# Kernel optimization log

Hardware: AMD Instinct MI355X
Metric: run time of the kernel (lower is better)

The kernel has to match this reference:

```python
import jax, jax.numpy as jnp
import numpy as np

B, S, H = 4, 2048, 2048
E, K = 8, 2


def setup_inputs() -> dict:
    key = jax.random.key(0)
    k1, k2, k3 = jax.random.split(key, 3)
    hidden_states = jax.random.normal(k1, (B, S, H), dtype=jnp.float32)
    # torch nn.Linear weight layout: [out_features, in_features]
    gate_w = jax.random.normal(k2, (E, H), dtype=jnp.float32) * (1.0 / np.sqrt(H))
    expert_w = jax.random.normal(k3, (E, H, H), dtype=jnp.float32) * (1.0 / np.sqrt(H))
    return {"hidden_states": hidden_states, "gate_w": gate_w, "expert_w": expert_w}


def reference(hidden_states, gate_w, expert_w):
    b, s, h = hidden_states.shape
    x = hidden_states.reshape(-1, h)                      # [T, H]
    T = x.shape[0]
    router_logits = x @ gate_w.T                          # [T, E]
    probs = jax.nn.softmax(router_logits.astype(jnp.float32), axis=-1)
    topk_w, topk_idx = jax.lax.top_k(probs, K)            # [T, K]
    topk_w = topk_w / jnp.sum(topk_w, axis=-1, keepdims=True)  # norm_topk_prob
    topk_w = topk_w.astype(x.dtype)
    # dense combine weights: cw[t, e] = sum_k topk_w[t, k] * (topk_idx[t, k] == e)
    cw = jnp.zeros((T, E), dtype=x.dtype).at[jnp.arange(T)[:, None], topk_idx].add(topk_w)
    # per-expert outputs: expert e computes x @ W_e^T  (W_e is [out, in])
    expert_out = jnp.einsum('th,edh->ted', x, expert_w)   # [T, E, H]
    out = jnp.einsum('ted,te->td', expert_out, cw)        # [T, H]
    return out.reshape(b, s, h), router_logits
```

## Files before the change

### kernel.cpp

```cpp
#include <hip/hip_runtime.h>
#include <hip/hip_bf16.h>

#define T_TOK 8192
#define H_DIM 2048
#define NE 8

typedef float f32x4 __attribute__((ext_vector_type(4)));
typedef short s16x8 __attribute__((ext_vector_type(8)));

typedef __attribute__((address_space(3))) unsigned int lds_uint;
typedef __attribute__((address_space(1))) const unsigned int glob_uint;

static __device__ __forceinline__ void async_ld16(const void* g, void* l) {
    __builtin_amdgcn_global_load_lds((glob_uint*)g, (lds_uint*)l, 16, 0, 0);
}

static __device__ __forceinline__ unsigned short f32_to_bf16(float f) {
    unsigned int u = __builtin_bit_cast(unsigned int, f);
    unsigned int r = (u + 0x7FFFu + ((u >> 16) & 1u)) >> 16;
    return (unsigned short)r;
}

__global__ __launch_bounds__(256) void prep_kernel(
        const float* __restrict__ w, unsigned short* __restrict__ wb,
        int* __restrict__ cnt) {
    const long g = (long)blockIdx.x * 256 + threadIdx.x;
    if (g < NE) cnt[g] = 0;
    const long nt = (long)gridDim.x * 256;
    const long N_W4 = (long)NE * H_DIM * H_DIM / 4;
    const float4* w4 = (const float4*)w;
    ushort4* wb4 = (ushort4*)wb;
    for (long i = g; i < N_W4; i += nt) {
        float4 v = w4[i];
        wb4[i] = make_ushort4(f32_to_bf16(v.x), f32_to_bf16(v.y),
                              f32_to_bf16(v.z), f32_to_bf16(v.w));
    }
}

__global__ __launch_bounds__(256) void router_kernel(
        const float* __restrict__ x, const float* __restrict__ gate,
        unsigned short* __restrict__ xb, float* __restrict__ logits,
        int* __restrict__ cnt, int* __restrict__ list, float* __restrict__ wl) {
    __shared__ float4 gs[NE * H_DIM / 4];
    __shared__ int aExp[32];
    __shared__ float aW[32];
    const float4* g4 = (const float4*)gate;
    for (int i = threadIdx.x; i < NE * H_DIM / 4; i += 256) gs[i] = g4[i];
    __syncthreads();

    const int wave = threadIdx.x >> 6, lane = threadIdx.x & 63;

    for (int it = 0; it < 4; ++it) {
        const int tok = wave * 4 + it;
        const int t = blockIdx.x * 16 + tok;
        const float4* xr = (const float4*)(x + (long)t * H_DIM);
        ushort4* xw = (ushort4*)(xb + (long)t * H_DIM);
        float acc[NE];
#pragma unroll
        for (int e = 0; e < NE; ++e) acc[e] = 0.f;
#pragma unroll
        for (int i = 0; i < 8; ++i) {
            float4 xv = xr[i * 64 + lane];
            xw[i * 64 + lane] = make_ushort4(f32_to_bf16(xv.x), f32_to_bf16(xv.y),
                                             f32_to_bf16(xv.z), f32_to_bf16(xv.w));
#pragma unroll
            for (int e = 0; e < NE; ++e) {
                float4 gv = gs[e * 512 + i * 64 + lane];
                acc[e] += xv.x * gv.x + xv.y * gv.y + xv.z * gv.z + xv.w * gv.w;
            }
        }
#pragma unroll
        for (int e = 0; e < NE; ++e)
#pragma unroll
            for (int off = 32; off > 0; off >>= 1)
                acc[e] += __shfl_xor(acc[e], off, 64);

        if (lane == 0) {
            float l0 = -1e30f; int i0 = 0;
#pragma unroll
            for (int e = 0; e < NE; ++e)
                if (acc[e] > l0) { l0 = acc[e]; i0 = e; }
            float l1 = -1e30f; int i1 = 0;
#pragma unroll
            for (int e = 0; e < NE; ++e)
                if (e != i0 && acc[e] > l1) { l1 = acc[e]; i1 = e; }
            float e1v = __expf(l1 - l0);
            float inv = 1.f / (1.f + e1v);
#pragma unroll
            for (int e = 0; e < NE; ++e) logits[(long)t * NE + e] = acc[e];
            aExp[tok * 2] = i0;     aW[tok * 2] = inv;
            aExp[tok * 2 + 1] = i1; aW[tok * 2 + 1] = e1v * inv;
        }
    }
    __syncthreads();

    if (threadIdx.x < NE) {
        const int e = threadIdx.x;
        int c = 0;
#pragma unroll
        for (int k = 0; k < 32; ++k) c += (aExp[k] == e);
        if (c) {
            int pos = atomicAdd(&cnt[e], c);
            for (int k = 0; k < 32; ++k)
                if (aExp[k] == e) {
                    list[e * T_TOK + pos] = blockIdx.x * 16 + (k >> 1);
                    wl[e * T_TOK + pos] = aW[k];
                    ++pos;
                }
        }
    }
}

__global__ __launch_bounds__(256, 4) void moe_gemm(
        const unsigned short* __restrict__ xb, const unsigned short* __restrict__ wb,
        const int* __restrict__ cnt, const int* __restrict__ list,
        const float* __restrict__ wl, float* __restrict__ out) {
    __shared__ uint4 As[1024];
    __shared__ uint4 Bs[1024];
    __shared__ int tIdx[128];
    __shared__ float tw[128];

    const int bx = blockIdx.x;
    const int e  = bx >> 10;
    const int rt = (bx >> 4) & 63;
    const int ct = bx & 15;
    const int n = cnt[e];
    const int row0 = rt << 7;
    if (row0 >= n) return;
    const int rv = min(128, n - row0);

    const int tid = threadIdx.x;
    if (tid < 128) {
        if (tid < rv) {
            tIdx[tid] = list[e * T_TOK + row0 + tid];
            tw[tid]   = wl[e * T_TOK + row0 + tid];
        } else { tIdx[tid] = 0; tw[tid] = 0.f; }
    }
    __syncthreads();

    const int wave = tid >> 6, lane = tid & 63;
    const int wm = (wave >> 1) << 6;
    const int wn = (wave & 1) << 6;
    const int quad = lane >> 4, l16 = lane & 15;

    f32x4 acc[4][4];
#pragma unroll
    for (int i = 0; i < 4; ++i)
#pragma unroll
        for (int j = 0; j < 4; ++j) acc[i][j] = (f32x4){0.f, 0.f, 0.f, 0.f};

    const unsigned short* aSrc[4];
    const unsigned short* bSrc[4];
    const long wbase = (long)e * H_DIM * H_DIM + (long)(ct * 128) * H_DIM;
#pragma unroll
    for (int i = 0; i < 4; ++i) {
        const int p = i * 256 + wave * 64 + lane;
        const int r = p >> 3;
        const int c = (p & 7) ^ (r & 7);
        aSrc[i] = xb + (long)tIdx[r] * H_DIM + c * 8;
        bSrc[i] = wb + wbase + (long)r * H_DIM + c * 8;
    }

    for (int kt = 0; kt < H_DIM / 64; ++kt) {
        const int k0 = kt * 64;
#pragma unroll
        for (int i = 0; i < 4; ++i) {
            async_ld16(aSrc[i] + k0, &As[i * 256 + wave * 64]);
            async_ld16(bSrc[i] + k0, &Bs[i * 256 + wave * 64]);
        }
        __syncthreads();
#pragma unroll
        for (int ks = 0; ks < 2; ++ks) {
            s16x8 af[4], bfr[4];
            const int kc = ks * 4 + quad;
#pragma unroll
            for (int i = 0; i < 4; ++i) {
                int r = wm + i * 16 + l16;
                af[i] = ((const s16x8*)As)[(r << 3) | (kc ^ (r & 7))];
            }
#pragma unroll
            for (int j = 0; j < 4; ++j) {
                int d = wn + j * 16 + l16;
                bfr[j] = ((const s16x8*)Bs)[(d << 3) | (kc ^ (d & 7))];
            }
#pragma unroll
            for (int i = 0; i < 4; ++i)
#pragma unroll
                for (int j = 0; j < 4; ++j)
                    acc[i][j] = __builtin_amdgcn_mfma_f32_16x16x32_bf16(
                        af[i], bfr[j], acc[i][j], 0, 0, 0);
        }
        __syncthreads();
    }

    const int colbase = ct * 128 + wn;
#pragma unroll
    for (int i = 0; i < 4; ++i) {
        const int rbase = wm + i * 16 + quad * 4;
#pragma unroll
        for (int jr = 0; jr < 4; ++jr) {
            const int r = rbase + jr;
            if (r < rv) {
                const float wgt = tw[r];
                const long orow = (long)tIdx[r] * H_DIM + colbase;
#pragma unroll
                for (int j = 0; j < 4; ++j)
                    atomicAdd(&out[orow + j * 16 + l16], acc[i][j][jr] * wgt);
            }
        }
    }
}

extern "C" void kernel_launch(void* const* d_in, const int* in_sizes, int n_in,
                              void* d_out, int out_size, void* d_ws, size_t ws_size,
                              hipStream_t stream) {
    (void)in_sizes; (void)n_in; (void)out_size; (void)ws_size;
    const float* x    = (const float*)d_in[0];
    const float* gate = (const float*)d_in[1];
    const float* w    = (const float*)d_in[2];

    float* out    = (float*)d_out;
    float* logits = out + (size_t)T_TOK * H_DIM;

    char* ws = (char*)d_ws;
    unsigned short* xb = (unsigned short*)(ws);
    unsigned short* wb = (unsigned short*)(ws + 33554432);
    int*   cnt  = (int*)(ws + 100663296);
    int*   list = (int*)(ws + 100663328);
    float* wl   = (float*)(ws + 100925472);

    hipMemsetAsync(out, 0, (size_t)T_TOK * H_DIM * sizeof(float), stream);
    prep_kernel<<<2048, 256, 0, stream>>>(w, wb, cnt);
    router_kernel<<<512, 256, 0, stream>>>(x, gate, xb, logits, cnt, list, wl);
    moe_gemm<<<8192, 256, 0, stream>>>(xb, wb, cnt, list, wl, out);
}
```

Baseline: 489.1 us.

## Enlarge MoE GEMM tile to 256x256 with double-buffered LDS pipeline

The grouped expert GEMM now uses 512-thread blocks computing 256x256 output tiles instead of 128x128, with double-buffered LDS and async prefetch of the next K-slice issued during the current slice's compute. Compute is split into four MFMA phases with interleaved fragment loads, s_setprio raising priority around the MFMA bursts, and explicit vmcnt waits replacing full syncthreads. The goal is more data reuse per LDS byte and hiding global-load latency behind MFMA work. The cost is more registers and LDS per block (lower occupancy), and more padding waste on partially filled expert row tiles.

Result: slower. 903.5 us (+84.7%).

```diff
diff --git a/kernel.cpp b/kernel.cpp
--- a/kernel.cpp
+++ b/kernel.cpp
@@ -4,6 +4,7 @@
 #define T_TOK 8192
 #define H_DIM 2048
 #define NE 8
+#define NT (H_DIM / 64)
 
 typedef float f32x4 __attribute__((ext_vector_type(4)));
 typedef short s16x8 __attribute__((ext_vector_type(8)));
@@ -111,26 +112,26 @@
     }
 }
 
-__global__ __launch_bounds__(256, 4) void moe_gemm(
+__global__ __launch_bounds__(512, 2) void moe_gemm(
         const unsigned short* __restrict__ xb, const unsigned short* __restrict__ wb,
         const int* __restrict__ cnt, const int* __restrict__ list,
         const float* __restrict__ wl, float* __restrict__ out) {
-    __shared__ uint4 As[1024];
-    __shared__ uint4 Bs[1024];
-    __shared__ int tIdx[128];
-    __shared__ float tw[128];
+    __shared__ uint4 Abuf[2][2048];
+    __shared__ uint4 Bbuf[2][2048];
+    __shared__ int tIdx[256];
+    __shared__ float tw[256];
 
     const int bx = blockIdx.x;
-    const int e  = bx >> 10;
-    const int rt = (bx >> 4) & 63;
-    const int ct = bx & 15;
+    const int e  = bx >> 8;
+    const int ct = (bx >> 5) & 7;
+    const int rt = bx & 31;
     const int n = cnt[e];
-    const int row0 = rt << 7;
+    const int row0 = rt << 8;
     if (row0 >= n) return;
-    const int rv = min(128, n - row0);
+    const int rv = min(256, n - row0);
 
     const int tid = threadIdx.x;
-    if (tid < 128) {
+    if (tid < 256) {
         if (tid < rv) {
             tIdx[tid] = list[e * T_TOK + row0 + tid];
             tw[tid]   = wl[e * T_TOK + row0 + tid];
@@ -139,64 +140,150 @@
     __syncthreads();
 
     const int wave = tid >> 6, lane = tid & 63;
-    const int wm = (wave >> 1) << 6;
-    const int wn = (wave & 1) << 6;
+    const int wm = wave >> 2;
+    const int wn = wave & 3;
     const int quad = lane >> 4, l16 = lane & 15;
 
-    f32x4 acc[4][4];
-#pragma unroll
-    for (int i = 0; i < 4; ++i)
+    f32x4 acc[8][4];
+#pragma unroll
+    for (int i = 0; i < 8; ++i)
 #pragma unroll
         for (int j = 0; j < 4; ++j) acc[i][j] = (f32x4){0.f, 0.f, 0.f, 0.f};
 
     const unsigned short* aSrc[4];
     const unsigned short* bSrc[4];
-    const long wbase = (long)e * H_DIM * H_DIM + (long)(ct * 128) * H_DIM;
+    const long wbase = (long)e * H_DIM * H_DIM + (long)(ct * 256) * H_DIM;
 #pragma unroll
     for (int i = 0; i < 4; ++i) {
-        const int p = i * 256 + wave * 64 + lane;
+        const int p = i * 512 + tid;
         const int r = p >> 3;
         const int c = (p & 7) ^ (r & 7);
         aSrc[i] = xb + (long)tIdx[r] * H_DIM + c * 8;
         bSrc[i] = wb + wbase + (long)r * H_DIM + c * 8;
     }
-
-    for (int kt = 0; kt < H_DIM / 64; ++kt) {
-        const int k0 = kt * 64;
-#pragma unroll
-        for (int i = 0; i < 4; ++i) {
-            async_ld16(aSrc[i] + k0, &As[i * 256 + wave * 64]);
-            async_ld16(bSrc[i] + k0, &Bs[i * 256 + wave * 64]);
-        }
-        __syncthreads();
+    uint4* const Ab = &Abuf[0][0];
+    uint4* const Bb = &Bbuf[0][0];
+    const int dst0 = wave * 64;
+
+#pragma unroll
+    for (int i = 0; i < 4; ++i) async_ld16(aSrc[i], Ab + i * 512 + dst0);
+#pragma unroll
+    for (int i = 0; i < 4; ++i) async_ld16(bSrc[i], Bb + i * 512 + dst0);
+
+    s16x8 Afr[4][2];
+    s16x8 Bfr[2][2][2];
+
+#pragma unroll 2
+    for (int t = 0; t < NT; ++t) {
+        const int b = t & 1;
+        const s16x8* Ap = (const s16x8*)(Ab + (b << 11));
+        const s16x8* Bp = (const s16x8*)(Bb + (b << 11));
+        uint4* An = Ab + ((b ^ 1) << 11);
+        uint4* Bn = Bb + ((b ^ 1) << 11);
+        const int k1 = (t + 1) << 6;
+
+        if (t + 1 < NT) {
+#pragma unroll
+            for (int i = 0; i < 4; ++i) async_ld16(aSrc[i] + k1, An + i * 512 + dst0);
+#pragma unroll
+            for (int i = 0; i < 2; ++i) async_ld16(bSrc[i] + k1, Bn + i * 512 + dst0);
+            asm volatile("s_waitcnt vmcnt(6)" ::: "memory");
+        } else {
+            asm volatile("s_waitcnt vmcnt(0)" ::: "memory");
+        }
+        __builtin_amdgcn_s_barrier();
+
 #pragma unroll
         for (int ks = 0; ks < 2; ++ks) {
-            s16x8 af[4], bfr[4];
             const int kc = ks * 4 + quad;
 #pragma unroll
             for (int i = 0; i < 4; ++i) {
-                int r = wm + i * 16 + l16;
-                af[i] = ((const s16x8*)As)[(r << 3) | (kc ^ (r & 7))];
-            }
-#pragma unroll
-            for (int j = 0; j < 4; ++j) {
-                int d = wn + j * 16 + l16;
-                bfr[j] = ((const s16x8*)Bs)[(d << 3) | (kc ^ (d & 7))];
-            }
+                const int r = wm * 128 + i * 16 + l16;
+                Afr[i][ks] = Ap[(r << 3) | (kc ^ (r & 7))];
+            }
+#pragma unroll
+            for (int j = 0; j < 2; ++j) {
+                const int d = wn * 64 + j * 16 + l16;
+                Bfr[0][j][ks] = Bp[(d << 3) | (kc ^ (d & 7))];
+            }
+        }
+        if (t + 1 < NT) {
+#pragma unroll
+            for (int i = 2; i < 4; ++i) async_ld16(bSrc[i] + k1, Bn + i * 512 + dst0);
+        }
+        __builtin_amdgcn_s_barrier();
+        __builtin_amdgcn_s_setprio(1);
+#pragma unroll
+        for (int ks = 0; ks < 2; ++ks)
 #pragma unroll
             for (int i = 0; i < 4; ++i)
 #pragma unroll
-                for (int j = 0; j < 4; ++j)
+                for (int j = 0; j < 2; ++j)
                     acc[i][j] = __builtin_amdgcn_mfma_f32_16x16x32_bf16(
-                        af[i], bfr[j], acc[i][j], 0, 0, 0);
-        }
-        __syncthreads();
-    }
-
-    const int colbase = ct * 128 + wn;
-#pragma unroll
-    for (int i = 0; i < 4; ++i) {
-        const int rbase = wm + i * 16 + quad * 4;
+                        Afr[i][ks], Bfr[0][j][ks], acc[i][j], 0, 0, 0);
+        __builtin_amdgcn_s_setprio(0);
+        __builtin_amdgcn_s_barrier();
+
+#pragma unroll
+        for (int ks = 0; ks < 2; ++ks) {
+            const int kc = ks * 4 + quad;
+#pragma unroll
+            for (int j = 0; j < 2; ++j) {
+                const int d = wn * 64 + 32 + j * 16 + l16;
+                Bfr[1][j][ks] = Bp[(d << 3) | (kc ^ (d & 7))];
+            }
+        }
+        __builtin_amdgcn_s_barrier();
+        __builtin_amdgcn_s_setprio(1);
+#pragma unroll
+        for (int ks = 0; ks < 2; ++ks)
+#pragma unroll
+            for (int i = 0; i < 4; ++i)
+#pragma unroll
+                for (int j = 0; j < 2; ++j)
+                    acc[i][2 + j] = __builtin_amdgcn_mfma_f32_16x16x32_bf16(
+                        Afr[i][ks], Bfr[1][j][ks], acc[i][2 + j], 0, 0, 0);
+        __builtin_amdgcn_s_setprio(0);
+        __builtin_amdgcn_s_barrier();
+
+#pragma unroll
+        for (int ks = 0; ks < 2; ++ks) {
+            const int kc = ks * 4 + quad;
+#pragma unroll
+            for (int i = 0; i < 4; ++i) {
+                const int r = wm * 128 + 64 + i * 16 + l16;
+                Afr[i][ks] = Ap[(r << 3) | (kc ^ (r & 7))];
+            }
+        }
+        __builtin_amdgcn_s_barrier();
+        __builtin_amdgcn_s_setprio(1);
+#pragma unroll
+        for (int ks = 0; ks < 2; ++ks)
+#pragma unroll
+            for (int i = 0; i < 4; ++i)
+#pragma unroll
+                for (int j = 0; j < 2; ++j)
+                    acc[4 + i][j] = __builtin_amdgcn_mfma_f32_16x16x32_bf16(
+                        Afr[i][ks], Bfr[0][j][ks], acc[4 + i][j], 0, 0, 0);
+        __builtin_amdgcn_s_setprio(0);
+        __builtin_amdgcn_s_barrier();
+
+        __builtin_amdgcn_s_setprio(1);
+#pragma unroll
+        for (int ks = 0; ks < 2; ++ks)
+#pragma unroll
+            for (int i = 0; i < 4; ++i)
+#pragma unroll
+                for (int j = 0; j < 2; ++j)
+                    acc[4 + i][2 + j] = __builtin_amdgcn_mfma_f32_16x16x32_bf16(
+                        Afr[i][ks], Bfr[1][j][ks], acc[4 + i][2 + j], 0, 0, 0);
+        __builtin_amdgcn_s_setprio(0);
+    }
+
+    const int colbase = ct * 256 + wn * 64;
+#pragma unroll
+    for (int mi = 0; mi < 8; ++mi) {
+        const int rbase = wm * 128 + mi * 16 + quad * 4;
 #pragma unroll
         for (int jr = 0; jr < 4; ++jr) {
             const int r = rbase + jr;
@@ -204,8 +291,8 @@
                 const float wgt = tw[r];
                 const long orow = (long)tIdx[r] * H_DIM + colbase;
 #pragma unroll
-                for (int j = 0; j < 4; ++j)
-                    atomicAdd(&out[orow + j * 16 + l16], acc[i][j][jr] * wgt);
+                for (int nj = 0; nj < 4; ++nj)
+                    atomicAdd(&out[orow + nj * 16 + l16], acc[mi][nj][jr] * wgt);
             }
         }
     }
@@ -232,5 +319,5 @@
     hipMemsetAsync(out, 0, (size_t)T_TOK * H_DIM * sizeof(float), stream);
     prep_kernel<<<2048, 256, 0, stream>>>(w, wb, cnt);
     router_kernel<<<512, 256, 0, stream>>>(x, gate, xb, logits, cnt, list, wl);
-    moe_gemm<<<8192, 256, 0, stream>>>(xb, wb, cnt, list, wl, out);
-}
+    moe_gemm<<<2048, 512, 0, stream>>>(xb, wb, cnt, list, wl, out);
+}
```

## Double-buffer LDS tiles in MoE GEMM with explicit vmcnt waits

Applied to the files above, without the earlier changes.

Converts the MoE GEMM's single-buffered LDS loop into a two-stage pipeline. The next k-tile is prefetched with global_load_lds into the alternate buffer while MFMAs run on the current one, and explicit s_waitcnt vmcnt and s_barrier replace __syncthreads. It also raises wave priority around the MFMA block and lowers the occupancy hint from 4 to 2 blocks per CU, since LDS use doubles to 64KB per block. This is meant to hide global-load latency, at the cost of fewer resident blocks and reliance on exact vmcnt accounting.

Result: slower. 503.6 us (+3.0%).

```diff
diff --git a/kernel.cpp b/kernel.cpp
--- a/kernel.cpp
+++ b/kernel.cpp
@@ -4,6 +4,7 @@
 #define T_TOK 8192
 #define H_DIM 2048
 #define NE 8
+#define NT (H_DIM / 64)
 
 typedef float f32x4 __attribute__((ext_vector_type(4)));
 typedef short s16x8 __attribute__((ext_vector_type(8)));
@@ -111,12 +112,12 @@
     }
 }
 
-__global__ __launch_bounds__(256, 4) void moe_gemm(
+__global__ __launch_bounds__(256, 2) void moe_gemm(
         const unsigned short* __restrict__ xb, const unsigned short* __restrict__ wb,
         const int* __restrict__ cnt, const int* __restrict__ list,
         const float* __restrict__ wl, float* __restrict__ out) {
-    __shared__ uint4 As[1024];
-    __shared__ uint4 Bs[1024];
+    __shared__ uint4 As[2][1024];
+    __shared__ uint4 Bs[2][1024];
     __shared__ int tIdx[128];
     __shared__ float tw[128];
 
@@ -154,21 +155,39 @@
     const long wbase = (long)e * H_DIM * H_DIM + (long)(ct * 128) * H_DIM;
 #pragma unroll
     for (int i = 0; i < 4; ++i) {
-        const int p = i * 256 + wave * 64 + lane;
+        const int p = i * 256 + tid;
         const int r = p >> 3;
         const int c = (p & 7) ^ (r & 7);
         aSrc[i] = xb + (long)tIdx[r] * H_DIM + c * 8;
         bSrc[i] = wb + wbase + (long)r * H_DIM + c * 8;
     }
-
-    for (int kt = 0; kt < H_DIM / 64; ++kt) {
-        const int k0 = kt * 64;
-#pragma unroll
-        for (int i = 0; i < 4; ++i) {
-            async_ld16(aSrc[i] + k0, &As[i * 256 + wave * 64]);
-            async_ld16(bSrc[i] + k0, &Bs[i * 256 + wave * 64]);
-        }
-        __syncthreads();
+    const int dst0 = wave * 64;
+
+#pragma unroll
+    for (int i = 0; i < 4; ++i) async_ld16(aSrc[i], &As[0][i * 256 + dst0]);
+#pragma unroll
+    for (int i = 0; i < 4; ++i) async_ld16(bSrc[i], &Bs[0][i * 256 + dst0]);
+
+#pragma unroll 2
+    for (int t = 0; t < NT; ++t) {
+        const int b = t & 1;
+
+        if (t + 1 < NT) {
+            const int k1 = (t + 1) << 6;
+#pragma unroll
+            for (int i = 0; i < 4; ++i)
+                async_ld16(aSrc[i] + k1, &As[b ^ 1][i * 256 + dst0]);
+#pragma unroll
+            for (int i = 0; i < 4; ++i)
+                async_ld16(bSrc[i] + k1, &Bs[b ^ 1][i * 256 + dst0]);
+            asm volatile("s_waitcnt vmcnt(8)" ::: "memory");
+        } else {
+            asm volatile("s_waitcnt vmcnt(0)" ::: "memory");
+        }
+        __builtin_amdgcn_s_barrier();
+
+        const s16x8* Ap = (const s16x8*)&As[b][0];
+        const s16x8* Bp = (const s16x8*)&Bs[b][0];
 #pragma unroll
         for (int ks = 0; ks < 2; ++ks) {
             s16x8 af[4], bfr[4];
@@ -176,21 +195,23 @@
 #pragma unroll
             for (int i = 0; i < 4; ++i) {
                 int r = wm + i * 16 + l16;
-                af[i] = ((const s16x8*)As)[(r << 3) | (kc ^ (r & 7))];
+                af[i] = Ap[(r << 3) | (kc ^ (r & 7))];
             }
 #pragma unroll
             for (int j = 0; j < 4; ++j) {
                 int d = wn + j * 16 + l16;
-                bfr[j] = ((const s16x8*)Bs)[(d << 3) | (kc ^ (d & 7))];
-            }
+                bfr[j] = Bp[(d << 3) | (kc ^ (d & 7))];
+            }
+            __builtin_amdgcn_s_setprio(1);
 #pragma unroll
             for (int i = 0; i < 4; ++i)
 #pragma unroll
                 for (int j = 0; j < 4; ++j)
                     acc[i][j] = __builtin_amdgcn_mfma_f32_16x16x32_bf16(
                         af[i], bfr[j], acc[i][j], 0, 0, 0);
-        }
-        __syncthreads();
+            __builtin_amdgcn_s_setprio(0);
+        }
+        __builtin_amdgcn_s_barrier();
     }
 
     const int colbase = ct * 128 + wn;
```

## Fuse router, weight conversion and output zeroing; remap GEMM blocks by XCD

Applied to the files above, without the earlier changes.

Merges the router, the fp32-to-bf16 weight conversion and the output zeroing into a single heterogeneous launch, with block ranges assigned to each role. The weight conversion now handles 8 elements per thread with 16-byte stores. The expert GEMM block index is remapped so consecutive tiles of the same expert land on the same XCD for better L2 reuse. This removes two launches and the full-output memset, but the router blocks now compete with the bandwidth-heavy conversion blocks.

New measurement: 520.4 us. +6.4%, slower.

```diff
diff --git a/kernel.cpp b/kernel.cpp
--- a/kernel.cpp
+++ b/kernel.cpp
@@ -21,38 +21,64 @@
     return (unsigned short)r;
 }
 
-__global__ __launch_bounds__(256) void prep_kernel(
-        const float* __restrict__ w, unsigned short* __restrict__ wb,
-        int* __restrict__ cnt) {
-    const long g = (long)blockIdx.x * 256 + threadIdx.x;
-    if (g < NE) cnt[g] = 0;
-    const long nt = (long)gridDim.x * 256;
-    const long N_W4 = (long)NE * H_DIM * H_DIM / 4;
-    const float4* w4 = (const float4*)w;
-    ushort4* wb4 = (ushort4*)wb;
-    for (long i = g; i < N_W4; i += nt) {
-        float4 v = w4[i];
-        wb4[i] = make_ushort4(f32_to_bf16(v.x), f32_to_bf16(v.y),
-                              f32_to_bf16(v.z), f32_to_bf16(v.w));
-    }
-}
-
-__global__ __launch_bounds__(256) void router_kernel(
+static __device__ __forceinline__ unsigned int pack_bf16x2(float lo, float hi) {
+    return (unsigned int)f32_to_bf16(lo) | ((unsigned int)f32_to_bf16(hi) << 16);
+}
+
+#define RT_NB 512
+#define PREP_NB 2048
+#define ZERO_NB 1024
+
+__global__ __launch_bounds__(256) void pre_kernel(
         const float* __restrict__ x, const float* __restrict__ gate,
-        unsigned short* __restrict__ xb, float* __restrict__ logits,
+        const float* __restrict__ w,
+        unsigned short* __restrict__ xb, unsigned short* __restrict__ wb,
+        float* __restrict__ logits, float* __restrict__ out,
         int* __restrict__ cnt, int* __restrict__ list, float* __restrict__ wl) {
     __shared__ float4 gs[NE * H_DIM / 4];
     __shared__ int aExp[32];
     __shared__ float aW[32];
+
+    const int bx = blockIdx.x;
+    const int tid = threadIdx.x;
+
+    if (bx >= RT_NB) {
+        if (bx < RT_NB + PREP_NB) {
+            const long g = (long)(bx - RT_NB) * 256 + tid;
+            const long nt = (long)PREP_NB * 256;
+            const long N8 = (long)NE * H_DIM * H_DIM / 8;
+            const float4* w4 = (const float4*)w;
+            uint4* wb4 = (uint4*)wb;
+            for (long i = g; i < N8; i += nt) {
+                float4 a = w4[i * 2];
+                float4 b = w4[i * 2 + 1];
+                uint4 o;
+                o.x = pack_bf16x2(a.x, a.y);
+                o.y = pack_bf16x2(a.z, a.w);
+                o.z = pack_bf16x2(b.x, b.y);
+                o.w = pack_bf16x2(b.z, b.w);
+                wb4[i] = o;
+            }
+        } else {
+            const long g = (long)(bx - RT_NB - PREP_NB) * 256 + tid;
+            const long nt = (long)ZERO_NB * 256;
+            const long N4 = (long)T_TOK * H_DIM / 4;
+            uint4* o4 = (uint4*)out;
+            const uint4 z = {0u, 0u, 0u, 0u};
+            for (long i = g; i < N4; i += nt) o4[i] = z;
+        }
+        return;
+    }
+
     const float4* g4 = (const float4*)gate;
-    for (int i = threadIdx.x; i < NE * H_DIM / 4; i += 256) gs[i] = g4[i];
+    for (int i = tid; i < NE * H_DIM / 4; i += 256) gs[i] = g4[i];
     __syncthreads();
 
-    const int wave = threadIdx.x >> 6, lane = threadIdx.x & 63;
+    const int wave = tid >> 6, lane = tid & 63;
 
     for (int it = 0; it < 4; ++it) {
         const int tok = wave * 4 + it;
-        const int t = blockIdx.x * 16 + tok;
+        const int t = bx * 16 + tok;
         const float4* xr = (const float4*)(x + (long)t * H_DIM);
         ushort4* xw = (ushort4*)(xb + (long)t * H_DIM);
         float acc[NE];
@@ -94,8 +120,8 @@
     }
     __syncthreads();
 
-    if (threadIdx.x < NE) {
-        const int e = threadIdx.x;
+    if (tid < NE) {
+        const int e = tid;
         int c = 0;
 #pragma unroll
         for (int k = 0; k < 32; ++k) c += (aExp[k] == e);
@@ -103,7 +129,7 @@
             int pos = atomicAdd(&cnt[e], c);
             for (int k = 0; k < 32; ++k)
                 if (aExp[k] == e) {
-                    list[e * T_TOK + pos] = blockIdx.x * 16 + (k >> 1);
+                    list[e * T_TOK + pos] = bx * 16 + (k >> 1);
                     wl[e * T_TOK + pos] = aW[k];
                     ++pos;
                 }
@@ -120,10 +146,15 @@
     __shared__ int tIdx[128];
     __shared__ float tw[128];
 
-    const int bx = blockIdx.x;
-    const int e  = bx >> 10;
-    const int rt = (bx >> 4) & 63;
-    const int ct = bx & 15;
+    const int b0 = blockIdx.x;
+    const int xcd  = b0 & 7;
+    const int slot = b0 >> 3;
+    const int chunk = xcd * 64 + (slot >> 4);
+    const int wg = (chunk << 4) | (slot & 15);
+
+    const int e  = wg >> 10;
+    const int rt = (wg >> 4) & 63;
+    const int ct = wg & 15;
     const int n = cnt[e];
     const int row0 = rt << 7;
     if (row0 >= n) return;
@@ -229,8 +260,8 @@
     int*   list = (int*)(ws + 100663328);
     float* wl   = (float*)(ws + 100925472);
 
-    hipMemsetAsync(out, 0, (size_t)T_TOK * H_DIM * sizeof(float), stream);
-    prep_kernel<<<2048, 256, 0, stream>>>(w, wb, cnt);
-    router_kernel<<<512, 256, 0, stream>>>(x, gate, xb, logits, cnt, list, wl);
+    hipMemsetAsync(cnt, 0, NE * sizeof(int), stream);
+    pre_kernel<<<RT_NB + PREP_NB + ZERO_NB, 256, 0, stream>>>(
+        x, gate, w, xb, wb, logits, out, cnt, list, wl);
     moe_gemm<<<8192, 256, 0, stream>>>(xb, wb, cnt, list, wl, out);
 }
```
